# Optimization experiments

Hardware: AMD Instinct MI355X
Metric: run time of the kernel (lower is better)

The kernel has to match this reference:

```python
import jax, jax.numpy as jnp
import numpy as np

DIM = 2048
NUM_HEADS = 16
HEAD_DIM = 128
SEQ = 4096
HDIM = NUM_HEADS * HEAD_DIM
EPS = 1e-6


def _rope_tables(seq_len, head_dim):
    quarter = head_dim // 4
    ang = (1.0 / 1024.0) ** np.linspace(0.0, 1.0, quarter, dtype=np.float32)
    ang = np.concatenate([ang, np.zeros(quarter, dtype=np.float32)])  # [head_dim//2]
    theta = np.arange(seq_len, dtype=np.float32)[:, None] * ang[None, :]  # [T, D/2]
    return jnp.asarray(np.cos(theta)), jnp.asarray(np.sin(theta))


def _rms_norm(x):
    return x * jax.lax.rsqrt(jnp.mean(x * x, axis=-1, keepdims=True) + EPS)


def _apply_rope(x, cos, sin):
    # x: [B, T, H, D]; cos/sin: [T, D/2]
    c = cos[None, :, None, :]
    s = sin[None, :, None, :]
    x1, x2 = jnp.split(x, 2, axis=-1)
    return jnp.concatenate([x1 * c + x2 * s, -x1 * s + x2 * c], axis=-1)


def setup_inputs() -> dict:
    key = jax.random.key(0)
    k1, k2, k3, k4, k5 = jax.random.split(key, 5)
    x = jax.random.normal(k1, (1, SEQ, DIM), dtype=jnp.float32)
    ve = jax.random.normal(k2, (1, SEQ, HDIM), dtype=jnp.float32)
    lambdas = jax.random.uniform(k3, (2,), dtype=jnp.float32)
    bound = (3.0 ** 0.5) * 0.5 * DIM ** (-0.5)
    qkv_w = jax.random.uniform(k4, (3, HDIM, DIM), dtype=jnp.float32, minval=-bound, maxval=bound)
    proj_w = 0.02 * jax.random.normal(k5, (DIM, HDIM), dtype=jnp.float32)
    return {"x": x, "ve": ve, "lambdas": lambdas, "qkv_w": qkv_w, "proj_w": proj_w}


def reference(x, ve, lambdas, qkv_w, proj_w):
    B, T, _ = x.shape
    cos, sin = _rope_tables(T, HEAD_DIM)
    # fused QKV projection: qkv_w [3, hdim, dim]
    qkv = jnp.einsum('btd,ced->cbte', x, qkv_w)  # [3, B, T, hdim]
    q, k, v = [a.reshape(B, T, NUM_HEADS, HEAD_DIM) for a in qkv]
    q = _apply_rope(_rms_norm(q), cos, sin)
    k = _apply_rope(_rms_norm(k), cos, sin)
    v = lambdas[0] * v + lambdas[1] * ve.reshape(v.shape)
    # causal SDPA, default scale 1/sqrt(head_dim)
    scale = 1.0 / jnp.sqrt(jnp.float32(HEAD_DIM))
    scores = jnp.einsum('bthd,bshd->bhts', q, k) * scale  # [B, H, T, T]
    causal = jnp.tril(jnp.ones((T, T), dtype=bool))
    scores = jnp.where(causal[None, None], scores, jnp.float32(-1e30))
    probs = jax.nn.softmax(scores, axis=-1)
    out = jnp.einsum('bhts,bshd->bthd', probs, v).reshape(B, T, HDIM)
    return out @ proj_w.T
```

## Files before the change

kernel.cpp:

```cpp
#include <hip/hip_runtime.h>
#include <cstdint>
#include <cstddef>

constexpr int T_SEQ = 4096;
constexpr int NH    = 16;
constexpr int HD    = 128;
constexpr int DIM   = 2048;
constexpr int HDIM  = 2048;

typedef __attribute__((ext_vector_type(8)))  short  short8;
typedef __attribute__((ext_vector_type(4)))  float  f32x4;
typedef __attribute__((ext_vector_type(16))) float  f32x16;
typedef __attribute__((ext_vector_type(8)))  unsigned short u16x8;
typedef __attribute__((ext_vector_type(4)))  unsigned short u16x4;
typedef __attribute__((ext_vector_type(4)))  unsigned uint4v;
typedef __attribute__((ext_vector_type(2)))  int int2v;

__device__ __forceinline__ unsigned short f2bf(float f) {
  unsigned u = __float_as_uint(f);
  return (unsigned short)((u + 0x7FFFu + ((u >> 16) & 1u)) >> 16);
}
__device__ __forceinline__ float bf2f(unsigned short h) {
  return __uint_as_float(((unsigned)h) << 16);
}
__device__ __forceinline__ void gload_lds16(const void* g, void* l) {
  __builtin_amdgcn_global_load_lds((const __attribute__((address_space(1))) void*)g,
                                   (__attribute__((address_space(3))) void*)l, 16, 0, 0);
}
__device__ __forceinline__ int2v plswap(int a, int b) {
  return __builtin_amdgcn_permlane32_swap(a, b, false, false);
}
__device__ __forceinline__ void bar() {
  asm volatile("" ::: "memory");
  __builtin_amdgcn_s_barrier();
  asm volatile("" ::: "memory");
}
#define VMCNT(n) asm volatile("s_waitcnt vmcnt(" #n ")" ::: "memory")

__global__ __launch_bounds__(256) void prep_all(const float* __restrict__ x,
                                                const float* __restrict__ qkv_w,
                                                const float* __restrict__ proj_w,
                                                unsigned short* __restrict__ xb,
                                                unsigned short* __restrict__ wqb,
                                                unsigned short* __restrict__ pwb,
                                                float* __restrict__ cosT,
                                                float* __restrict__ sinT) {
  constexpr int N1 = T_SEQ * DIM / 4;
  constexpr int N2 = N1 + 3 * HDIM * DIM / 4;
  constexpr int N3 = N2 + DIM * HDIM / 4;
  int gid = blockIdx.x * 256 + threadIdx.x;
  const float* src; unsigned short* dst; int i4;
  if (gid < N1)      { src = x;      dst = xb;  i4 = gid; }
  else if (gid < N2) { src = qkv_w;  dst = wqb; i4 = gid - N1; }
  else if (gid < N3) { src = proj_w; dst = pwb; i4 = gid - N2; }
  else {
    int idx = gid - N3;
    int t = idx >> 6, i = idx & 63;
    float ang = (i < 32) ? exp2f(-10.0f * (float)i / 31.0f) : 0.0f;
    float th = (float)t * ang;
    cosT[idx] = cosf(th);
    sinT[idx] = sinf(th);
    return;
  }
  float4 v = ((const float4*)src)[i4];
  u16x4 o; o.x = f2bf(v.x); o.y = f2bf(v.y); o.z = f2bf(v.z); o.w = f2bf(v.w);
  ((u16x4*)dst)[i4] = o;
}

template <int MODE>
__global__ __launch_bounds__(512) void gemm256(const unsigned short* __restrict__ A,
                                               const unsigned short* __restrict__ B,
                                               int K, unsigned short* __restrict__ outb,
                                               float* __restrict__ outf, int N) {
  __shared__ __align__(16) char SM[3 * 49152];
  const int tid = threadIdx.x, w = tid >> 6, lane = tid & 63;
  const int wm = w >> 2, wn = w & 3;
  const int lr = lane >> 4, lc = lane & 15, lc7 = lc & 7;
  const int cpx = gridDim.x >> 3;
  const int idx = (blockIdx.x & 7) * cpx + (blockIdx.x >> 3);
  const int m0 = (idx & 31) * 128, n0 = (idx >> 5) * 256;

  const int arow = lane >> 3;
  const int xcol = ((lane & 7) ^ ((lane >> 3) & 7)) * 8;

  auto stageA = [&](int buf, int t) {
    char* base = SM + buf * 49152;
#pragma unroll
    for (int i = 0; i < 2; i++) {
      int c = w + i * 8;
      gload_lds16(A + (size_t)(m0 + c * 8 + arow) * K + t * 64 + xcol, base + c * 1024);
    }
  };
  auto stageB0 = [&](int buf, int t) {
    char* base = SM + buf * 49152 + 16384;
    gload_lds16(B + (size_t)(n0 + w * 8 + arow) * K + t * 64 + xcol, base + w * 1024);
  };
  auto stageB1 = [&](int buf, int t) {
    char* base = SM + buf * 49152 + 16384;
#pragma unroll
    for (int i = 1; i < 4; i++) {
      int c = w + i * 8;
      gload_lds16(B + (size_t)(n0 + c * 8 + arow) * K + t * 64 + xcol, base + c * 1024);
    }
  };

  f32x4 acc[4][4] = {};
  const int NT = K >> 6;

  stageA(0, 0); stageB0(0, 0); stageB1(0, 0);
  stageA(1, 1); stageB0(1, 1); stageB1(1, 1);
  VMCNT(6);
  bar();

#pragma unroll 1
  for (int t = 0; t < NT; t++) {
    const int c = t % 3, s = (t + 2) % 3;
    const bool st = (t + 2) < NT;
    const char* Ab = SM + c * 49152;
    const char* Bb = Ab + 16384;

    short8 a[4], b[4];
#pragma unroll
    for (int mi = 0; mi < 4; mi++)
      a[mi] = *(const short8*)(Ab + (wm * 64 + mi * 16 + lc) * 128 + ((0 + lr) ^ lc7) * 16);
#pragma unroll
    for (int ni = 0; ni < 4; ni++)
      b[ni] = *(const short8*)(Bb + (wn * 64 + ni * 16 + lc) * 128 + ((0 + lr) ^ lc7) * 16);
    if (st) { stageA(s, t + 2); stageB0(s, t + 2); }
    __builtin_amdgcn_s_setprio(1);
#pragma unroll
    for (int mi = 0; mi < 4; mi++)
#pragma unroll
      for (int ni = 0; ni < 4; ni++)
        acc[mi][ni] = __builtin_amdgcn_mfma_f32_16x16x32_bf16(a[mi], b[ni], acc[mi][ni], 0, 0, 0);
    __builtin_amdgcn_s_setprio(0);

#pragma unroll
    for (int mi = 0; mi < 4; mi++)
      a[mi] = *(const short8*)(Ab + (wm * 64 + mi * 16 + lc) * 128 + ((4 + lr) ^ lc7) * 16);
#pragma unroll
    for (int ni = 0; ni < 4; ni++)
      b[ni] = *(const short8*)(Bb + (wn * 64 + ni * 16 + lc) * 128 + ((4 + lr) ^ lc7) * 16);
    if (st) stageB1(s, t + 2);
    if (st) { VMCNT(6); } else { VMCNT(0); }
    bar();
    __builtin_amdgcn_s_setprio(1);
#pragma unroll
    for (int mi = 0; mi < 4; mi++)
#pragma unroll
      for (int ni = 0; ni < 4; ni++)
        acc[mi][ni] = __builtin_amdgcn_mfma_f32_16x16x32_bf16(a[mi], b[ni], acc[mi][ni], 0, 0, 0);
    __builtin_amdgcn_s_setprio(0);
    bar();
  }

#pragma unroll
  for (int mi = 0; mi < 4; mi++)
#pragma unroll
    for (int ni = 0; ni < 4; ni++)
#pragma unroll
      for (int r = 0; r < 4; r++) {
        int t = m0 + wm * 64 + mi * 16 + lr * 4 + r;
        int n = n0 + wn * 64 + ni * 16 + lc;
        float v = acc[mi][ni][r];
        if (MODE == 0) {
          int cc = n >> 11, e = n & 2047, h = e >> 7, d = e & 127;
          outb[(((size_t)cc * NH + h) * T_SEQ + t) * HD + d] = f2bf(v);
        } else {
          outf[(size_t)t * N + n] = v;
        }
      }
}

__global__ __launch_bounds__(256) void norm_vmix(const unsigned short* __restrict__ qkvb,
                                                 const float* __restrict__ cosT,
                                                 const float* __restrict__ sinT,
                                                 const float* __restrict__ ve,
                                                 const float* __restrict__ lam,
                                                 unsigned short* __restrict__ vt,
                                                 unsigned char* __restrict__ qk8) {
  __shared__ float tile[64][65];
  const int bid = blockIdx.x, tid = threadIdx.x;

  if (bid < 8192) {
    const int li = tid & 15;
    const int row = bid * 16 + (tid >> 4);
    const int t = row & (T_SEQ - 1);
    const unsigned short* rp = qkvb + (size_t)row * HD + li * 8;
    u16x8 raw = *(const u16x8*)rp;

    float v[8]; float ss = 0.0f;
#pragma unroll
    for (int j = 0; j < 8; j++) { v[j] = bf2f(raw[j]); ss += v[j] * v[j]; }
#pragma unroll
    for (int off = 1; off < 16; off <<= 1) ss += __shfl_xor(ss, off, 16);
    float rs = rsqrtf(ss * (1.0f / 128.0f) + 1e-6f);
    if (row < NH * T_SEQ) rs *= 0.088388347648318447f * 1.44269504f;

    uint4v rw = __builtin_bit_cast(uint4v, raw);
    uint4v pwv;
    pwv.x = (unsigned)__shfl_xor((int)rw.x, 8, 16);
    pwv.y = (unsigned)__shfl_xor((int)rw.y, 8, 16);
    pwv.z = (unsigned)__shfl_xor((int)rw.z, 8, 16);
    pwv.w = (unsigned)__shfl_xor((int)rw.w, 8, 16);
    u16x8 praw = __builtin_bit_cast(u16x8, pwv);
    float pv[8];
#pragma unroll
    for (int j = 0; j < 8; j++) pv[j] = bf2f(praw[j]);

    const int e0 = (li & 7) * 8;
    const bool hi8 = li >= 8;
    float4 c0 = *(const float4*)(cosT + t * 64 + e0);
    float4 c1 = *(const float4*)(cosT + t * 64 + e0 + 4);
    float4 s0 = *(const float4*)(sinT + t * 64 + e0);
    float4 s1 = *(const float4*)(sinT + t * 64 + e0 + 4);
    float cc[8] = {c0.x, c0.y, c0.z, c0.w, c1.x, c1.y, c1.z, c1.w};
    float sn[8] = {s0.x, s0.y, s0.z, s0.w, s1.x, s1.y, s1.z, s1.w};

    float rr[8];
#pragma unroll
    for (int j = 0; j < 8; j++) {
      float x1 = hi8 ? pv[j] : v[j];
      float x2 = hi8 ? v[j] : pv[j];
      float r = hi8 ? (-x1 * sn[j] + x2 * cc[j]) : (x1 * cc[j] + x2 * sn[j]);
      rr[j] = r * rs;
    }
    int w0 = 0, w1 = 0;
    w0 = __builtin_amdgcn_cvt_pk_fp8_f32(rr[0], rr[1], w0, false);
    w0 = __builtin_amdgcn_cvt_pk_fp8_f32(rr[2], rr[3], w0, true);
    w1 = __builtin_amdgcn_cvt_pk_fp8_f32(rr[4], rr[5], w1, false);
    w1 = __builtin_amdgcn_cvt_pk_fp8_f32(rr[6], rr[7], w1, true);
    int2v o8; o8.x = w0; o8.y = w1;
    *(int2v*)(qk8 + (size_t)row * HD + li * 8) = o8;
  } else {
    const int j2 = bid - 8192;
    const int t0 = (j2 & 63) * 64, d0 = ((j2 >> 6) & 1) * 64, h = j2 >> 7;
    const unsigned short* vb = qkvb + (size_t)2 * NH * T_SEQ * HD;
    const float l0 = lam[0], l1 = lam[1];
    const int tl = tid >> 4, dl4 = (tid & 15) * 4;
#pragma unroll
    for (int i = 0; i < 4; i++) {
      int t_local = tl + i * 16;
      int t = t0 + t_local;
      const unsigned short* vp = vb + ((size_t)h * T_SEQ + t) * HD + d0 + dl4;
      const float* vep = ve + (size_t)t * HDIM + h * HD + d0 + dl4;
      u16x4 vv = *(const u16x4*)vp;
      float4 vef = *(const float4*)vep;
      tile[t_local][dl4 + 0] = l0 * bf2f(vv.x) + l1 * vef.x;
      tile[t_local][dl4 + 1] = l0 * bf2f(vv.y) + l1 * vef.y;
      tile[t_local][dl4 + 2] = l0 * bf2f(vv.z) + l1 * vef.z;
      tile[t_local][dl4 + 3] = l0 * bf2f(vv.w) + l1 * vef.w;
    }
    __syncthreads();
#pragma unroll
    for (int i = 0; i < 2; i++) {
      int idx = tid + i * 256;
      int d_local = idx >> 3, tloc = (idx & 7) * 8;
      u16x8 o;
#pragma unroll
      for (int j = 0; j < 8; j++) o[j] = f2bf(tile[tloc + j][d_local]);
      *(u16x8*)(vt + ((size_t)h * HD + d0 + d_local) * T_SEQ + t0 + tloc) = o;
    }
  }
}

__global__ __launch_bounds__(512)
__attribute__((amdgpu_waves_per_eu(2, 2)))
void attn_fwd(const unsigned char* __restrict__ q8,
              const unsigned char* __restrict__ k8,
              const unsigned short* __restrict__ vt,
              unsigned short* __restrict__ ao) {
  __shared__ __align__(16) char SMEM[98304];
  __shared__ int gctr[2];
  const int bid = blockIdx.x;
  const int h  = (bid & 7) + ((bid >> 7) << 3);
  const int pr = (bid >> 3) & 15;
  const int tid = threadIdx.x, w = tid >> 6, lane = tid & 63;
  const int g = w >> 2, wq = w & 3;
  const int l31 = lane & 31, hi = lane >> 5, r7 = l31 & 7;
  const unsigned char* qh = q8 + (size_t)h * T_SEQ * HD;
  const unsigned char* kh = k8 + (size_t)h * T_SEQ * HD;
  const unsigned short* vh = vt + (size_t)h * HD * T_SEQ;

  if (tid < 2) gctr[tid] = 0;
  __syncthreads();
  int bcnt = 0;
  auto GBAR = [&]() {
    asm volatile("s_waitcnt lgkmcnt(0)" ::: "memory");
    ++bcnt;
    if (lane == 0)
      __hip_atomic_fetch_add(&gctr[g], 1, __ATOMIC_RELEASE, __HIP_MEMORY_SCOPE_WORKGROUP);
    while (__hip_atomic_load(&gctr[g], __ATOMIC_ACQUIRE, __HIP_MEMORY_SCOPE_WORKGROUP) < 4 * bcnt)
      __builtin_amdgcn_s_sleep(1);
  };

  char* Kbase = SMEM + g * 49152;
  char* Vbase = Kbase + 16384;

  const int vcrow = lane >> 3, vslot0 = lane & 7;

  auto STAGE = [&](int buf, int t) {
#pragma unroll
    for (int i = 0; i < 2; i++) {
      int c = wq * 2 + i;
      int r = c * 8 + (lane >> 3);
      int rsrc = (r & ~12) | ((r & 4) << 1) | ((r & 8) >> 1);
      int sl = ((lane & 7) ^ (r & 7)) * 16;
      gload_lds16(kh + (size_t)(t * 64 + rsrc) * HD + sl,
                  Kbase + buf * 8192 + c * 1024);
    }
#pragma unroll
    for (int i = 0; i < 4; i++) {
      int vrow = (wq * 4 + i) * 8 + vcrow;
      int vcol = (vslot0 ^ (vrow & 7)) * 8;
      gload_lds16(vh + (size_t)vrow * T_SEQ + t * 64 + vcol,
                  Vbase + buf * 16384 + (wq * 4 + i) * 1024);
    }
  };

  const float FM = 18.75f;

#pragma unroll 1
  for (int which = 0; which < 2; ++which) {
    const int qt = which ? pr : (31 - pr);
    const int ng = qt + 1;
    const int q_row = qt * 128 + wq * 32 + l31;

    long qf8[8];
#pragma unroll
    for (int dk = 0; dk < 8; dk++)
      qf8[dk] = *(const long*)(qh + (size_t)q_row * HD + dk * 16 + hi * 8);

    f32x16 accO[4] = {};
    float l_r = 0.0f;

    __syncthreads();
    STAGE(0, g);

#pragma unroll 1
    for (int it = 0; it < ng; it++) {
      const int t = 2 * it + g;
      const int cur = it & 1;
      asm volatile("s_waitcnt vmcnt(0)" ::: "memory");
      GBAR();
      if (it + 1 < ng) STAGE(cur ^ 1, t + 2);

      f32x16 accS0 = {}, accS1 = {};
      const char* Kb = Kbase + cur * 8192;
      __builtin_amdgcn_s_setprio(1);
#pragma unroll
      for (int dk = 0; dk < 8; dk++) {
        int off = l31 * 128 + ((dk ^ r7) * 16) + hi * 8;
        long k0 = *(const long*)(Kb + off);
        long k1 = *(const long*)(Kb + 32 * 128 + off);
        accS0 = __builtin_amdgcn_mfma_f32_32x32x16_fp8_fp8(k0, qf8[dk], accS0, 0, 0, 0);
        accS1 = __builtin_amdgcn_mfma_f32_32x32x16_fp8_fp8(k1, qf8[dk], accS1, 0, 0, 0);
      }
      __builtin_amdgcn_s_setprio(0);

      float p[32];
      const bool need_mask = (t * 64 + 63) > (qt * 128 + wq * 32);
      if (need_mask) {
#pragma unroll
        for (int r = 0; r < 16; r++) {
          int kv0 = t * 64 + (r & 7) + 8 * hi + 16 * (r >> 3);
          p[r]      = (kv0      > q_row) ? 0.0f : exp2f(accS0[r] - FM);
          p[16 + r] = (kv0 + 32 > q_row) ? 0.0f : exp2f(accS1[r] - FM);
        }
      } else {
#pragma unroll
        for (int r = 0; r < 16; r++) {
          p[r]      = exp2f(accS0[r] - FM);
          p[16 + r] = exp2f(accS1[r] - FM);
        }
      }

      float s16[16];
#pragma unroll
      for (int i = 0; i < 16; i++) s16[i] = p[i] + p[i + 16];
#pragma unroll
      for (int st = 8; st >= 1; st >>= 1)
#pragma unroll
        for (int i = 0; i < st; i++) s16[i] += s16[i + st];
      int2v sr_ = plswap(__float_as_int(s16[0]), __float_as_int(s16[0]));
      l_r += s16[0] + __int_as_float(hi ? sr_.x : sr_.y);

      const char* Vb = Vbase + cur * 16384 + l31 * 128;
#pragma unroll
      for (int ks = 0; ks < 4; ks++) {
        uint4v pw;
#pragma unroll
        for (int w2 = 0; w2 < 4; w2++) {
          unsigned pk_;
          asm("v_cvt_pk_bf16_f32 %0, %1, %2"
              : "=v"(pk_) : "v"(p[8 * ks + 2 * w2]), "v"(p[8 * ks + 2 * w2 + 1]));
          pw[w2] = pk_;
        }
        short8 pb = __builtin_bit_cast(short8, pw);
        int sl = ((2 * ks + hi) ^ r7) * 16;
        __builtin_amdgcn_s_setprio(1);
#pragma unroll
        for (int dt = 0; dt < 4; dt++) {
          short8 vf = *(const short8*)(Vb + dt * 32 * 128 + sl);
          accO[dt] = __builtin_amdgcn_mfma_f32_32x32x16_bf16(vf, pb, accO[dt], 0, 0, 0);
        }
        __builtin_amdgcn_s_setprio(0);
      }
    }

    __syncthreads();
    float* SM_acc = (float*)(SMEM + 32768);
    float* SM_l   = (float*)SMEM;
    const int q_local = wq * 32 + l31;
    if (g == 1) {
#pragma unroll
      for (int dt = 0; dt < 4; dt++)
#pragma unroll
        for (int r = 0; r < 16; r++) {
          int d = 32 * dt + (r & 3) + 8 * (r >> 2) + 4 * hi;
          SM_acc[q_local * 128 + (d ^ l31)] = accO[dt][r];
        }
      if (hi == 0) SM_l[q_local] = l_r;
    }
    __syncthreads();
    if (g == 0) {
      float lo = SM_l[q_local];
      float inv = 1.0f / (l_r + lo);
#pragma unroll
      for (int dt = 0; dt < 4; dt++)
#pragma unroll
        for (int q4 = 0; q4 < 4; q4++) {
          int dbase = 32 * dt + 8 * q4 + 4 * hi;
          u16x4 o;
#pragma unroll
          for (int j = 0; j < 4; j++) {
            int r = q4 * 4 + j, d = dbase + j;
            float vo = SM_acc[q_local * 128 + (d ^ l31)];
            o[j] = f2bf((accO[dt][r] + vo) * inv);
          }
          *(u16x4*)(ao + (size_t)q_row * HDIM + h * HD + dbase) = o;
        }
    }
  }
}

extern "C" void kernel_launch(void* const* d_in, const int* in_sizes, int n_in,
                              void* d_out, int out_size, void* d_ws, size_t ws_size,
                              hipStream_t stream) {
  const float* x      = (const float*)d_in[0];
  const float* ve     = (const float*)d_in[1];
  const float* lam    = (const float*)d_in[2];
  const float* qkv_w  = (const float*)d_in[3];
  const float* proj_w = (const float*)d_in[4];
  float* out = (float*)d_out;

  char* p = (char*)d_ws;
  float* cosT = (float*)p;            p += (size_t)T_SEQ * 64 * 4;
  float* sinT = (float*)p;            p += (size_t)T_SEQ * 64 * 4;
  unsigned short* xb   = (unsigned short*)p; p += (size_t)T_SEQ * DIM * 2;
  unsigned short* wqb  = (unsigned short*)p; p += (size_t)3 * HDIM * DIM * 2;
  unsigned short* pwb  = (unsigned short*)p; p += (size_t)DIM * HDIM * 2;
  unsigned short* qkvb = (unsigned short*)p; p += (size_t)3 * NH * T_SEQ * HD * 2;
  unsigned short* vtb  = (unsigned short*)p; p += (size_t)NH * HD * T_SEQ * 2;
  unsigned short* aob  = (unsigned short*)p; p += (size_t)T_SEQ * HDIM * 2;
  unsigned char*  qk8  = (unsigned char*)p;  p += (size_t)2 * NH * T_SEQ * HD;

  constexpr int PREP_N = T_SEQ * DIM / 4 + 3 * HDIM * DIM / 4 + DIM * HDIM / 4 + T_SEQ * 64;
  prep_all<<<PREP_N / 256, 256, 0, stream>>>(x, qkv_w, proj_w, xb, wqb, pwb, cosT, sinT);

  gemm256<0><<<768, 512, 0, stream>>>(xb, wqb, DIM, qkvb, nullptr, 3 * HDIM);
  norm_vmix<<<10240, 256, 0, stream>>>(qkvb, cosT, sinT, ve, lam, vtb, qk8);
  attn_fwd<<<256, 512, 0, stream>>>(qk8, qk8 + (size_t)NH * T_SEQ * HD, vtb, aob);
  gemm256<1><<<256, 512, 0, stream>>>(aob, pwb, HDIM, nullptr, out, HDIM);
}
```

Measured before the change: 281.1 us.

## Fuse QK RMSNorm, RoPE and FP8 quantization into the QKV GEMM epilogue

The QKV GEMM now stages its fp32 accumulator tile in shared memory for Q and K column blocks, then applies RMS norm, RoPE and the softmax scale, and writes FP8 directly. This drops the bf16 round trip of Q and K through global memory and the separate normalization launch. The V path still writes bf16 and goes to a slimmer mix-and-transpose kernel. The cost is a longer, more serial epilogue in the GEMM, with an extra barrier and shared-memory staging. Normalization now works on fp32 accumulators instead of bf16-rounded values, which changes numerics slightly.

```diff
diff --git a/kernel.cpp b/kernel.cpp
--- a/kernel.cpp
+++ b/kernel.cpp
@@ -67,11 +67,12 @@
   ((u16x4*)dst)[i4] = o;
 }
 
-template <int MODE>
-__global__ __launch_bounds__(512) void gemm256(const unsigned short* __restrict__ A,
-                                               const unsigned short* __restrict__ B,
-                                               int K, unsigned short* __restrict__ outb,
-                                               float* __restrict__ outf, int N) {
+__global__ __launch_bounds__(512) void gemm_qkv(const unsigned short* __restrict__ A,
+                                                const unsigned short* __restrict__ B,
+                                                const float* __restrict__ cosT,
+                                                const float* __restrict__ sinT,
+                                                unsigned char* __restrict__ qk8,
+                                                unsigned short* __restrict__ vb) {
   __shared__ __align__(16) char SM[3 * 49152];
   const int tid = threadIdx.x, w = tid >> 6, lane = tid & 63;
   const int wm = w >> 2, wn = w & 3;
@@ -79,6 +80,7 @@
   const int cpx = gridDim.x >> 3;
   const int idx = (blockIdx.x & 7) * cpx + (blockIdx.x >> 3);
   const int m0 = (idx & 31) * 128, n0 = (idx >> 5) * 256;
+  constexpr int K = DIM;
 
   const int arow = lane >> 3;
   const int xcol = ((lane & 7) ^ ((lane >> 3) & 7)) * 8;
@@ -154,6 +156,169 @@
     bar();
   }
 
+  const int cc = n0 >> 11;
+  if (cc < 2) {
+    float* TL = (float*)SM;
+#pragma unroll
+    for (int mi = 0; mi < 4; mi++)
+#pragma unroll
+      for (int ni = 0; ni < 4; ni++)
+#pragma unroll
+        for (int r = 0; r < 4; r++)
+          TL[(wm * 64 + mi * 16 + lr * 4 + r) * 260 + wn * 64 + ni * 16 + lc] =
+              acc[mi][ni][r];
+    bar();
+
+    const int h0 = (n0 & 2047) >> 7;
+    const int li = tid & 15, grp = tid >> 4;
+    const bool hi8 = li >= 8;
+    const int e0 = (li & 7) * 8;
+#pragma unroll 1
+    for (int itr = 0; itr < 8; itr++) {
+      int rr = itr * 32 + grp;
+      int hh = rr >> 7, tl2 = rr & 127;
+      int tg = m0 + tl2;
+      const float* rowp = TL + tl2 * 260 + hh * 128;
+      f32x4 a4 = *(const f32x4*)(rowp + li * 8);
+      f32x4 b4 = *(const f32x4*)(rowp + li * 8 + 4);
+      float v[8];
+#pragma unroll
+      for (int j = 0; j < 4; j++) { v[j] = a4[j]; v[4 + j] = b4[j]; }
+      float ss = 0.0f;
+#pragma unroll
+      for (int j = 0; j < 8; j++) ss += v[j] * v[j];
+#pragma unroll
+      for (int off = 1; off < 16; off <<= 1) ss += __shfl_xor(ss, off, 16);
+      float rs = rsqrtf(ss * (1.0f / 128.0f) + 1e-6f);
+      if (cc == 0) rs *= 0.088388347648318447f * 1.44269504f;
+
+      float pv[8];
+#pragma unroll
+      for (int j = 0; j < 8; j++) pv[j] = __shfl_xor(v[j], 8, 16);
+
+      float4 c0 = *(const float4*)(cosT + tg * 64 + e0);
+      float4 c1 = *(const float4*)(cosT + tg * 64 + e0 + 4);
+      float4 s0 = *(const float4*)(sinT + tg * 64 + e0);
+      float4 s1 = *(const float4*)(sinT + tg * 64 + e0 + 4);
+      float ct[8] = {c0.x, c0.y, c0.z, c0.w, c1.x, c1.y, c1.z, c1.w};
+      float sn[8] = {s0.x, s0.y, s0.z, s0.w, s1.x, s1.y, s1.z, s1.w};
+
+      float rr8[8];
+#pragma unroll
+      for (int j = 0; j < 8; j++) {
+        float x1 = hi8 ? pv[j] : v[j];
+        float x2 = hi8 ? v[j] : pv[j];
+        float r = hi8 ? (-x1 * sn[j] + x2 * ct[j]) : (x1 * ct[j] + x2 * sn[j]);
+        rr8[j] = r * rs;
+      }
+      int w0 = 0, w1 = 0;
+      w0 = __builtin_amdgcn_cvt_pk_fp8_f32(rr8[0], rr8[1], w0, false);
+      w0 = __builtin_amdgcn_cvt_pk_fp8_f32(rr8[2], rr8[3], w0, true);
+      w1 = __builtin_amdgcn_cvt_pk_fp8_f32(rr8[4], rr8[5], w1, false);
+      w1 = __builtin_amdgcn_cvt_pk_fp8_f32(rr8[6], rr8[7], w1, true);
+      int2v o8; o8.x = w0; o8.y = w1;
+      *(int2v*)(qk8 + ((size_t)(cc * NH + h0 + hh) * T_SEQ + tg) * HD + li * 8) = o8;
+    }
+  } else {
+#pragma unroll
+    for (int mi = 0; mi < 4; mi++)
+#pragma unroll
+      for (int ni = 0; ni < 4; ni++)
+#pragma unroll
+        for (int r = 0; r < 4; r++) {
+          int t = m0 + wm * 64 + mi * 16 + lr * 4 + r;
+          int n = n0 + wn * 64 + ni * 16 + lc;
+          int e = n & 2047, h = e >> 7, d = e & 127;
+          vb[((size_t)h * T_SEQ + t) * HD + d] = f2bf(acc[mi][ni][r]);
+        }
+  }
+}
+
+__global__ __launch_bounds__(512) void gemm256(const unsigned short* __restrict__ A,
+                                               const unsigned short* __restrict__ B,
+                                               int K, float* __restrict__ outf, int N) {
+  __shared__ __align__(16) char SM[3 * 49152];
+  const int tid = threadIdx.x, w = tid >> 6, lane = tid & 63;
+  const int wm = w >> 2, wn = w & 3;
+  const int lr = lane >> 4, lc = lane & 15, lc7 = lc & 7;
+  const int cpx = gridDim.x >> 3;
+  const int idx = (blockIdx.x & 7) * cpx + (blockIdx.x >> 3);
+  const int m0 = (idx & 31) * 128, n0 = (idx >> 5) * 256;
+
+  const int arow = lane >> 3;
+  const int xcol = ((lane & 7) ^ ((lane >> 3) & 7)) * 8;
+
+  auto stageA = [&](int buf, int t) {
+    char* base = SM + buf * 49152;
+#pragma unroll
+    for (int i = 0; i < 2; i++) {
+      int c = w + i * 8;
+      gload_lds16(A + (size_t)(m0 + c * 8 + arow) * K + t * 64 + xcol, base + c * 1024);
+    }
+  };
+  auto stageB0 = [&](int buf, int t) {
+    char* base = SM + buf * 49152 + 16384;
+    gload_lds16(B + (size_t)(n0 + w * 8 + arow) * K + t * 64 + xcol, base + w * 1024);
+  };
+  auto stageB1 = [&](int buf, int t) {
+    char* base = SM + buf * 49152 + 16384;
+#pragma unroll
+    for (int i = 1; i < 4; i++) {
+      int c = w + i * 8;
+      gload_lds16(B + (size_t)(n0 + c * 8 + arow) * K + t * 64 + xcol, base + c * 1024);
+    }
+  };
+
+  f32x4 acc[4][4] = {};
+  const int NT = K >> 6;
+
+  stageA(0, 0); stageB0(0, 0); stageB1(0, 0);
+  stageA(1, 1); stageB0(1, 1); stageB1(1, 1);
+  VMCNT(6);
+  bar();
+
+#pragma unroll 1
+  for (int t = 0; t < NT; t++) {
+    const int c = t % 3, s = (t + 2) % 3;
+    const bool st = (t + 2) < NT;
+    const char* Ab = SM + c * 49152;
+    const char* Bb = Ab + 16384;
+
+    short8 a[4], b[4];
+#pragma unroll
+    for (int mi = 0; mi < 4; mi++)
+      a[mi] = *(const short8*)(Ab + (wm * 64 + mi * 16 + lc) * 128 + ((0 + lr) ^ lc7) * 16);
+#pragma unroll
+    for (int ni = 0; ni < 4; ni++)
+      b[ni] = *(const short8*)(Bb + (wn * 64 + ni * 16 + lc) * 128 + ((0 + lr) ^ lc7) * 16);
+    if (st) { stageA(s, t + 2); stageB0(s, t + 2); }
+    __builtin_amdgcn_s_setprio(1);
+#pragma unroll
+    for (int mi = 0; mi < 4; mi++)
+#pragma unroll
+      for (int ni = 0; ni < 4; ni++)
+        acc[mi][ni] = __builtin_amdgcn_mfma_f32_16x16x32_bf16(a[mi], b[ni], acc[mi][ni], 0, 0, 0);
+    __builtin_amdgcn_s_setprio(0);
+
+#pragma unroll
+    for (int mi = 0; mi < 4; mi++)
+      a[mi] = *(const short8*)(Ab + (wm * 64 + mi * 16 + lc) * 128 + ((4 + lr) ^ lc7) * 16);
+#pragma unroll
+    for (int ni = 0; ni < 4; ni++)
+      b[ni] = *(const short8*)(Bb + (wn * 64 + ni * 16 + lc) * 128 + ((4 + lr) ^ lc7) * 16);
+    if (st) stageB1(s, t + 2);
+    if (st) { VMCNT(6); } else { VMCNT(0); }
+    bar();
+    __builtin_amdgcn_s_setprio(1);
+#pragma unroll
+    for (int mi = 0; mi < 4; mi++)
+#pragma unroll
+      for (int ni = 0; ni < 4; ni++)
+        acc[mi][ni] = __builtin_amdgcn_mfma_f32_16x16x32_bf16(a[mi], b[ni], acc[mi][ni], 0, 0, 0);
+    __builtin_amdgcn_s_setprio(0);
+    bar();
+  }
+
 #pragma unroll
   for (int mi = 0; mi < 4; mi++)
 #pragma unroll
@@ -162,105 +327,42 @@
       for (int r = 0; r < 4; r++) {
         int t = m0 + wm * 64 + mi * 16 + lr * 4 + r;
         int n = n0 + wn * 64 + ni * 16 + lc;
-        float v = acc[mi][ni][r];
-        if (MODE == 0) {
-          int cc = n >> 11, e = n & 2047, h = e >> 7, d = e & 127;
-          outb[(((size_t)cc * NH + h) * T_SEQ + t) * HD + d] = f2bf(v);
-        } else {
-          outf[(size_t)t * N + n] = v;
-        }
+        outf[(size_t)t * N + n] = acc[mi][ni][r];
       }
 }
 
-__global__ __launch_bounds__(256) void norm_vmix(const unsigned short* __restrict__ qkvb,
-                                                 const float* __restrict__ cosT,
-                                                 const float* __restrict__ sinT,
-                                                 const float* __restrict__ ve,
-                                                 const float* __restrict__ lam,
-                                                 unsigned short* __restrict__ vt,
-                                                 unsigned char* __restrict__ qk8) {
+__global__ __launch_bounds__(256) void vmix_transpose(const unsigned short* __restrict__ vb,
+                                                      const float* __restrict__ ve,
+                                                      const float* __restrict__ lam,
+                                                      unsigned short* __restrict__ vt) {
   __shared__ float tile[64][65];
-  const int bid = blockIdx.x, tid = threadIdx.x;
-
-  if (bid < 8192) {
-    const int li = tid & 15;
-    const int row = bid * 16 + (tid >> 4);
-    const int t = row & (T_SEQ - 1);
-    const unsigned short* rp = qkvb + (size_t)row * HD + li * 8;
-    u16x8 raw = *(const u16x8*)rp;
-
-    float v[8]; float ss = 0.0f;
-#pragma unroll
-    for (int j = 0; j < 8; j++) { v[j] = bf2f(raw[j]); ss += v[j] * v[j]; }
-#pragma unroll
-    for (int off = 1; off < 16; off <<= 1) ss += __shfl_xor(ss, off, 16);
-    float rs = rsqrtf(ss * (1.0f / 128.0f) + 1e-6f);
-    if (row < NH * T_SEQ) rs *= 0.088388347648318447f * 1.44269504f;
-
-    uint4v rw = __builtin_bit_cast(uint4v, raw);
-    uint4v pwv;
-    pwv.x = (unsigned)__shfl_xor((int)rw.x, 8, 16);
-    pwv.y = (unsigned)__shfl_xor((int)rw.y, 8, 16);
-    pwv.z = (unsigned)__shfl_xor((int)rw.z, 8, 16);
-    pwv.w = (unsigned)__shfl_xor((int)rw.w, 8, 16);
-    u16x8 praw = __builtin_bit_cast(u16x8, pwv);
-    float pv[8];
-#pragma unroll
-    for (int j = 0; j < 8; j++) pv[j] = bf2f(praw[j]);
-
-    const int e0 = (li & 7) * 8;
-    const bool hi8 = li >= 8;
-    float4 c0 = *(const float4*)(cosT + t * 64 + e0);
-    float4 c1 = *(const float4*)(cosT + t * 64 + e0 + 4);
-    float4 s0 = *(const float4*)(sinT + t * 64 + e0);
-    float4 s1 = *(const float4*)(sinT + t * 64 + e0 + 4);
-    float cc[8] = {c0.x, c0.y, c0.z, c0.w, c1.x, c1.y, c1.z, c1.w};
-    float sn[8] = {s0.x, s0.y, s0.z, s0.w, s1.x, s1.y, s1.z, s1.w};
-
-    float rr[8];
-#pragma unroll
-    for (int j = 0; j < 8; j++) {
-      float x1 = hi8 ? pv[j] : v[j];
-      float x2 = hi8 ? v[j] : pv[j];
-      float r = hi8 ? (-x1 * sn[j] + x2 * cc[j]) : (x1 * cc[j] + x2 * sn[j]);
-      rr[j] = r * rs;
-    }
-    int w0 = 0, w1 = 0;
-    w0 = __builtin_amdgcn_cvt_pk_fp8_f32(rr[0], rr[1], w0, false);
-    w0 = __builtin_amdgcn_cvt_pk_fp8_f32(rr[2], rr[3], w0, true);
-    w1 = __builtin_amdgcn_cvt_pk_fp8_f32(rr[4], rr[5], w1, false);
-    w1 = __builtin_amdgcn_cvt_pk_fp8_f32(rr[6], rr[7], w1, true);
-    int2v o8; o8.x = w0; o8.y = w1;
-    *(int2v*)(qk8 + (size_t)row * HD + li * 8) = o8;
-  } else {
-    const int j2 = bid - 8192;
-    const int t0 = (j2 & 63) * 64, d0 = ((j2 >> 6) & 1) * 64, h = j2 >> 7;
-    const unsigned short* vb = qkvb + (size_t)2 * NH * T_SEQ * HD;
-    const float l0 = lam[0], l1 = lam[1];
-    const int tl = tid >> 4, dl4 = (tid & 15) * 4;
-#pragma unroll
-    for (int i = 0; i < 4; i++) {
-      int t_local = tl + i * 16;
-      int t = t0 + t_local;
-      const unsigned short* vp = vb + ((size_t)h * T_SEQ + t) * HD + d0 + dl4;
-      const float* vep = ve + (size_t)t * HDIM + h * HD + d0 + dl4;
-      u16x4 vv = *(const u16x4*)vp;
-      float4 vef = *(const float4*)vep;
-      tile[t_local][dl4 + 0] = l0 * bf2f(vv.x) + l1 * vef.x;
-      tile[t_local][dl4 + 1] = l0 * bf2f(vv.y) + l1 * vef.y;
-      tile[t_local][dl4 + 2] = l0 * bf2f(vv.z) + l1 * vef.z;
-      tile[t_local][dl4 + 3] = l0 * bf2f(vv.w) + l1 * vef.w;
-    }
-    __syncthreads();
-#pragma unroll
-    for (int i = 0; i < 2; i++) {
-      int idx = tid + i * 256;
-      int d_local = idx >> 3, tloc = (idx & 7) * 8;
-      u16x8 o;
-#pragma unroll
-      for (int j = 0; j < 8; j++) o[j] = f2bf(tile[tloc + j][d_local]);
-      *(u16x8*)(vt + ((size_t)h * HD + d0 + d_local) * T_SEQ + t0 + tloc) = o;
-    }
+  const int tid = threadIdx.x;
+  const int j2 = blockIdx.x;
+  const int t0 = (j2 & 63) * 64, d0 = ((j2 >> 6) & 1) * 64, h = j2 >> 7;
+  const float l0 = lam[0], l1 = lam[1];
+  const int tl = tid >> 4, dl4 = (tid & 15) * 4;
+#pragma unroll
+  for (int i = 0; i < 4; i++) {
+    int t_local = tl + i * 16;
+    int t = t0 + t_local;
+    const unsigned short* vp = vb + ((size_t)h * T_SEQ + t) * HD + d0 + dl4;
+    const float* vep = ve + (size_t)t * HDIM + h * HD + d0 + dl4;
+    u16x4 vv = *(const u16x4*)vp;
+    float4 vef = *(const float4*)vep;
+    tile[t_local][dl4 + 0] = l0 * bf2f(vv.x) + l1 * vef.x;
+    tile[t_local][dl4 + 1] = l0 * bf2f(vv.y) + l1 * vef.y;
+    tile[t_local][dl4 + 2] = l0 * bf2f(vv.z) + l1 * vef.z;
+    tile[t_local][dl4 + 3] = l0 * bf2f(vv.w) + l1 * vef.w;
+  }
+  __syncthreads();
+#pragma unroll
+  for (int i = 0; i < 2; i++) {
+    int idx = tid + i * 256;
+    int d_local = idx >> 3, tloc = (idx & 7) * 8;
+    u16x8 o;
+#pragma unroll
+    for (int j = 0; j < 8; j++) o[j] = f2bf(tile[tloc + j][d_local]);
+    *(u16x8*)(vt + ((size_t)h * HD + d0 + d_local) * T_SEQ + t0 + tloc) = o;
   }
 }
 
@@ -460,7 +562,7 @@
   unsigned short* xb   = (unsigned short*)p; p += (size_t)T_SEQ * DIM * 2;
   unsigned short* wqb  = (unsigned short*)p; p += (size_t)3 * HDIM * DIM * 2;
   unsigned short* pwb  = (unsigned short*)p; p += (size_t)DIM * HDIM * 2;
-  unsigned short* qkvb = (unsigned short*)p; p += (size_t)3 * NH * T_SEQ * HD * 2;
+  unsigned short* vbuf = (unsigned short*)p; p += (size_t)NH * T_SEQ * HD * 2;
   unsigned short* vtb  = (unsigned short*)p; p += (size_t)NH * HD * T_SEQ * 2;
   unsigned short* aob  = (unsigned short*)p; p += (size_t)T_SEQ * HDIM * 2;
   unsigned char*  qk8  = (unsigned char*)p;  p += (size_t)2 * NH * T_SEQ * HD;
@@ -468,8 +570,8 @@
   constexpr int PREP_N = T_SEQ * DIM / 4 + 3 * HDIM * DIM / 4 + DIM * HDIM / 4 + T_SEQ * 64;
   prep_all<<<PREP_N / 256, 256, 0, stream>>>(x, qkv_w, proj_w, xb, wqb, pwb, cosT, sinT);
 
-  gemm256<0><<<768, 512, 0, stream>>>(xb, wqb, DIM, qkvb, nullptr, 3 * HDIM);
-  norm_vmix<<<10240, 256, 0, stream>>>(qkvb, cosT, sinT, ve, lam, vtb, qk8);
+  gemm_qkv<<<768, 512, 0, stream>>>(xb, wqb, cosT, sinT, qk8, vbuf);
+  vmix_transpose<<<2048, 256, 0, stream>>>(vbuf, ve, lam, vtb);
   attn_fwd<<<256, 512, 0, stream>>>(qk8, qk8 + (size_t)NH * T_SEQ * HD, vtb, aob);
-  gemm256<1><<<256, 512, 0, stream>>>(aob, pwb, HDIM, nullptr, out, HDIM);
-}
+  gemm256<<<256, 512, 0, stream>>>(aob, pwb, HDIM, out, HDIM);
+}
```

Result: faster. 272.6 us (-3.0%).
